# Kernel optimization log

Hardware: AMD Instinct MI355X
Metric: run time of the kernel (lower is better)

The kernel has to match this reference:

```python
import jax, jax.numpy as jnp
import numpy as np

N, E, R, F, HD = 4096, 2048, 4, 128, 256
DEG_EPS = 1e-8
BN_EPS = 1e-5
LN_EPS = 1e-5


def _xavier(k, shape):
    scale = np.sqrt(2.0 / (shape[-2] + shape[-1])).astype(np.float32)
    return jax.random.normal(k, shape, jnp.float32) * scale


def setup_inputs() -> dict:
    key = jax.random.key(0)
    ks = jax.random.split(key, 8)
    X = jax.random.normal(ks[0], (N, F), jnp.float32)
    # sparse binary incidence matrices, one per relation type, stacked [R,N,E]
    H = (jax.random.uniform(ks[1], (R, N, E)) < 0.05).astype(jnp.float32)
    return {
        "X": X,
        "H": H,
        "W1": _xavier(ks[2], (R, F, HD)),
        "W2": _xavier(ks[3], (R, HD, HD)),
        "W3": _xavier(ks[4], (R, HD, F)),
        "imp": jnp.ones((3, R), jnp.float32),        # relation_importance per conv layer
        "b1": jnp.zeros((HD,), jnp.float32),
        "b2": jnp.zeros((HD,), jnp.float32),
        "b3": jnp.zeros((F,), jnp.float32),
        "bn_gamma": jnp.ones((2, HD), jnp.float32),
        "bn_beta": jnp.zeros((2, HD), jnp.float32),
        "ln_gamma": jnp.ones((2, HD), jnp.float32),
        "ln_beta": jnp.zeros((2, HD), jnp.float32),
        "rel_attn": jnp.ones((R,), jnp.float32) / R,
    }


def typed_conv(X, Hw, W, imp, bias):
    # Hw: [R,N,E] weighted incidence; theta = Dv^{-1/2} H De^{-1/2} via row/col scaling
    dv = jnp.power(Hw.sum(axis=2) + DEG_EPS, -0.5)   # [R,N]
    de = jnp.power(Hw.sum(axis=1) + DEG_EPS, -0.5)   # [R,E]
    theta = Hw * dv[:, :, None] * de[:, None, :]     # [R,N,E]
    # (theta @ theta^T) @ X computed as theta @ (theta^T @ X) -- same math, no NxN
    t = jnp.einsum('rne,nf->ref', theta, X)          # [R,E,Fin]
    Hn = jnp.einsum('rne,ref->rnf', theta, t)        # [R,N,Fin]
    out = jnp.einsum('rnf,rfo->rno', Hn, W)          # [R,N,Fout]
    out = out * jax.nn.sigmoid(imp)[:, None, None]
    return out.sum(axis=0) + bias


def bn_ln_elu(X, bg, bb, lg, lb):
    # BatchNorm1d with batch statistics (biased var), then LayerNorm, then ELU
    mu = X.mean(axis=0)
    var = X.var(axis=0)
    X = (X - mu) * jax.lax.rsqrt(var + BN_EPS) * bg + bb
    m = X.mean(axis=-1, keepdims=True)
    v = X.var(axis=-1, keepdims=True)
    X = (X - m) * jax.lax.rsqrt(v + LN_EPS) * lg + lb
    return jax.nn.elu(X)


def reference(X, H, W1, W2, W3, imp, b1, b2, b3, bn_gamma, bn_beta, ln_gamma, ln_beta, rel_attn):
    rw = jax.nn.softmax(rel_attn)
    Hw = H * rw[:, None, None]                       # weighted incidence per relation
    h = typed_conv(X, Hw, W1, imp[0], b1)
    h = bn_ln_elu(h, bn_gamma[0], bn_beta[0], ln_gamma[0], ln_beta[0])
    h = typed_conv(h, Hw, W2, imp[1], b2)
    h = bn_ln_elu(h, bn_gamma[1], bn_beta[1], ln_gamma[1], ln_beta[1])
    out = typed_conv(h, Hw, W3, imp[2], b3)
    return out + X  # residual: out_channels == in_channels by construction
```

## Files before the change

kernel.cpp:

```cpp
#include <hip/hip_runtime.h>
#include <hip/hip_bf16.h>

#define NN 4096
#define EE 2048
#define RR 4
#define FF 128
#define HDD 256

typedef __attribute__((ext_vector_type(4))) float floatx4;
typedef __attribute__((ext_vector_type(8))) __bf16 bf16x8;

#define AS1 __attribute__((address_space(1)))
#define AS3 __attribute__((address_space(3)))

__device__ __forceinline__ void async16(const void* g, void* l) {
  __builtin_amdgcn_global_load_lds((const AS1 void*)(unsigned long long)(g),
                                   (AS3 void*)(unsigned int)(unsigned long long)(l),
                                   16, 0, 0);
}

__device__ inline unsigned short f2b(float x) {
  unsigned int u = __float_as_uint(x);
  unsigned int r = u + 0x7fffu + ((u >> 16) & 1u);
  return (unsigned short)(r >> 16);
}
__device__ inline float b2f(unsigned short u) { return __uint_as_float((unsigned int)u << 16); }

__device__ inline float rel_w(const float* rel, int r) {
  float m = fmaxf(fmaxf(rel[0], rel[1]), fmaxf(rel[2], rel[3]));
  float s = 0.f;
#pragma unroll
  for (int i = 0; i < RR; i++) s += expf(rel[i] - m);
  return expf(rel[r] - m) / s;
}

__global__ void k_prep1(const float* __restrict__ H, const float* __restrict__ rel,
                        const float* __restrict__ W1, const float* __restrict__ W2,
                        const float* __restrict__ W3, const float* __restrict__ imp,
                        float* __restrict__ dvs, unsigned long long* __restrict__ mask,
                        unsigned short* __restrict__ W1catT, unsigned short* __restrict__ W2T,
                        unsigned short* __restrict__ W3T, float* __restrict__ de, float* __restrict__ cs) {
  int b = blockIdx.x;
  if (b < 4096) {
    int wave = (b << 2) | (threadIdx.x >> 6);
    int lane = threadIdx.x & 63;
    int r = wave >> 12;
    const float* row = H + (size_t)wave * EE;
    unsigned long long* mrow = mask + (size_t)wave * (EE / 64);
    float s = 0.f;
    for (int j = 0; j < EE / 64; j++) {
      float h = row[j * 64 + lane];
      s += h;
      unsigned long long m = __ballot(h != 0.0f);
      if (lane == 0) mrow[j] = m;
    }
    for (int off = 32; off; off >>= 1) s += __shfl_down(s, off);
    if (lane == 0) {
      float rwr = rel_w(rel, r);
      dvs[wave] = rwr * rsqrtf(rwr * s + 1e-8f);
    }
  } else if (b < 4096 + 2048) {
    int idx = (b - 4096) * 256 + threadIdx.x;
    if (idx < RR * FF * HDD) {
      int o = idx % HDD, f = (idx / HDD) % FF, r = idx / (HDD * FF);
      float sg = 1.0f / (1.0f + expf(-imp[r]));
      W1catT[(size_t)o * (RR * FF) + r * FF + f] = f2b(sg * W1[((size_t)r * FF + f) * HDD + o]);
    } else if (idx < RR * FF * HDD + RR * HDD * HDD) {
      int j = idx - RR * FF * HDD;
      int c = j % HDD, o = (j / HDD) % HDD, r = j / (HDD * HDD);
      float sg = 1.0f / (1.0f + expf(-imp[RR + r]));
      W2T[j] = f2b(sg * W2[((size_t)r * HDD + c) * HDD + o]);
    } else {
      int j = idx - RR * FF * HDD - RR * HDD * HDD;
      int c = j % HDD, o = (j / HDD) % FF, r = j / (HDD * FF);
      float sg = 1.0f / (1.0f + expf(-imp[2 * RR + r]));
      W3T[j] = f2b(sg * W3[((size_t)r * HDD + c) * FF + o]);
    }
  } else {
    int i = (b - 6144) * 256 + threadIdx.x;
    if (i < RR * EE) de[i] = 0.f;
    else if (i < RR * EE + 2 * HDD) cs[i - RR * EE] = 0.f;
  }
}

__global__ void k_prep2(const unsigned long long* __restrict__ m1, unsigned long long* __restrict__ m2,
                        float* __restrict__ de, const float* __restrict__ X,
                        const float* __restrict__ dvs, unsigned short* __restrict__ XdvT) {
  __shared__ unsigned long long w[64 * 33];
  __shared__ unsigned short tile[64][65];
  int t = threadIdx.x;
  if (blockIdx.x < 256) {
    int r = blockIdx.x >> 6;
    int n0 = (blockIdx.x & 63) << 6;
    const unsigned long long* src = m1 + ((size_t)r * NN + n0) * 32;
#pragma unroll
    for (int i = 0; i < 8; i++) {
      int idx = t + i * 256;
      int n = idx >> 5, W = idx & 31;
      w[n * 33 + W] = src[idx];
    }
    __syncthreads();
    int wid = t >> 6, lane = t & 63;
    int v = n0 >> 6;
#pragma unroll
    for (int Wi = 0; Wi < 8; Wi++) {
      int W = wid * 8 + Wi;
      unsigned long long myw = w[lane * 33 + W];
      unsigned long long out = 0;
      for (int b = 0; b < 64; b++) {
        unsigned long long mm = __ballot(((myw >> b) & 1ULL) != 0);
        if (lane == b) out = mm;
      }
      m2[((size_t)r * EE + W * 64 + lane) * 64 + v] = out;
      atomicAdd(&de[r * EE + W * 64 + lane], (float)__popcll(out));
    }
  } else {
    int idx = blockIdx.x - 256;
    int c0 = (idx & 1) * 64, m0 = ((idx >> 1) & 63) * 64, r = idx >> 7;
    int tr = t >> 4, tc = t & 15;
#pragma unroll
    for (int i = 0; i < 4; i++) {
      int m = m0 + tr + 16 * i;
      float d = dvs[(size_t)r * NN + m];
      float4 v = *(const float4*)(X + (size_t)m * FF + c0 + tc * 4);
      tile[tr + 16 * i][tc * 4 + 0] = f2b(v.x * d);
      tile[tr + 16 * i][tc * 4 + 1] = f2b(v.y * d);
      tile[tr + 16 * i][tc * 4 + 2] = f2b(v.z * d);
      tile[tr + 16 * i][tc * 4 + 3] = f2b(v.w * d);
    }
    __syncthreads();
    unsigned short* db = XdvT + (size_t)r * FF * NN;
#pragma unroll
    for (int i = 0; i < 4; i++) {
      int c = c0 + tr + 16 * i;
      ushort4 v;
      v.x = tile[tc * 4 + 0][tr + 16 * i];
      v.y = tile[tc * 4 + 1][tr + 16 * i];
      v.z = tile[tc * 4 + 2][tr + 16 * i];
      v.w = tile[tc * 4 + 3][tr + 16 * i];
      *(ushort4*)(db + (size_t)c * NN + m0 + tc * 4) = v;
    }
  }
}

template <int DECA, int DECB>
__global__ __launch_bounds__(256) void k_gemm3(
    const unsigned short* __restrict__ A, const unsigned short* __restrict__ BT,
    int K, int SK, int lda, int ldb, long a_rs, long b_rs,
    unsigned short* __restrict__ P, long c_ps, long c_rs, int ldc,
    const unsigned long long* __restrict__ dm, int dnw, long drow_rs,
    const float* __restrict__ cscale, long cs_rs) {
  __shared__ unsigned short Al[2][128 * 64];
  __shared__ unsigned short Bl[2][128 * 64];
  int tid = threadIdx.x, wid = tid >> 6, lane = tid & 63;
  int m0 = blockIdx.x << 7, n0 = blockIdx.y << 7;
  int z = blockIdx.z, zr = z / SK, kz = z - zr * SK;
  int Kc = K / SK;
  int r8 = lane >> 3, c8 = lane & 7;
  int swz = ((c8 ^ r8) << 3);
  const unsigned short* Ab = A + (DECA ? 0 : ((size_t)zr * a_rs + (size_t)m0 * lda + (size_t)kz * Kc));
  const unsigned short* Bb = BT + (DECB ? 0 : ((size_t)zr * b_rs + (size_t)n0 * ldb + (size_t)kz * Kc));
  const unsigned int* mrow = nullptr;
  int drow = 0, dhalf = 0, dsw = 0;
  if (DECA || DECB) {
    drow = tid >> 1; dhalf = tid & 1;
    long mrowOff = (long)zr * drow_rs + (DECA ? m0 : n0) + drow;
    mrow = (const unsigned int*)(dm + (size_t)mrowOff * dnw);
    dsw = drow & 7;
  }
  auto stage = [&](int pb, int k0) {
    if (!DECA) {
#pragma unroll
      for (int t = 0; t < 4; t++) {
        int rbase = (wid << 5) + (t << 3);
        int row = rbase + r8;
        async16(Ab + (size_t)row * lda + k0 + swz, &Al[pb][rbase * 64 + lane * 8]);
      }
    }
    if (!DECB) {
#pragma unroll
      for (int t = 0; t < 4; t++) {
        int rbase = (wid << 5) + (t << 3);
        int row = rbase + r8;
        async16(Bb + (size_t)row * ldb + k0 + swz, &Bl[pb][rbase * 64 + lane * 8]);
      }
    }
    if (DECA || DECB) {
      unsigned short* Dl = DECA ? &Al[pb][0] : &Bl[pb][0];
      long kglob = (long)kz * Kc + k0;
      unsigned int bits = mrow[(kglob >> 5) + dhalf];
      uint4 zz = {0u, 0u, 0u, 0u};
#pragma unroll
      for (int g = 0; g < 4; g++) {
        int chunk = ((dhalf << 2) | g) ^ dsw;
        *(uint4*)&Dl[drow * 64 + chunk * 8] = zz;
      }
      while (bits) {
        int b = __builtin_ctz(bits);
        bits &= bits - 1;
        int kl = (dhalf << 5) + b;
        Dl[drow * 64 + (((kl >> 3) ^ dsw) << 3) + (kl & 7)] = (unsigned short)0x3F80;
      }
    }
  };
  int wm = (wid >> 1) << 6, wn = (wid & 1) << 6;
  int fm = lane & 15, quad = lane >> 4;
  int f7 = fm & 7;
  floatx4 acc[4][4];
#pragma unroll
  for (int i = 0; i < 4; i++)
#pragma unroll
    for (int j = 0; j < 4; j++) acc[i][j] = (floatx4){0.f, 0.f, 0.f, 0.f};
  auto compute = [&](int pb) {
#pragma unroll
    for (int ks = 0; ks < 2; ks++) {
      int kg = (ks << 2) | quad;
      int ko = ((kg ^ f7) << 3);
      bf16x8 a[4], b[4];
#pragma unroll
      for (int i = 0; i < 4; i++) {
        a[i] = *(const bf16x8*)&Al[pb][(wm + i * 16 + fm) * 64 + ko];
        b[i] = *(const bf16x8*)&Bl[pb][(wn + i * 16 + fm) * 64 + ko];
      }
#pragma unroll
      for (int i = 0; i < 4; i++)
#pragma unroll
        for (int j = 0; j < 4; j++)
          acc[i][j] = __builtin_amdgcn_mfma_f32_16x16x32_bf16(a[i], b[j], acc[i][j], 0, 0, 0);
    }
  };
  stage(0, 0);
  __syncthreads();
  for (int k0 = 0; k0 < Kc; k0 += 128) {
    if (k0 + 64 < Kc) stage(1, k0 + 64);
    compute(0);
    __syncthreads();
    if (k0 + 128 < Kc) stage(0, k0 + 128);
    compute(1);
    __syncthreads();
  }
  unsigned short* Cb = P + (size_t)kz * c_ps + (size_t)zr * c_rs;
  float csc[4];
#pragma unroll
  for (int ni = 0; ni < 4; ni++)
    csc[ni] = cscale ? cscale[(size_t)zr * cs_rs + n0 + wn + ni * 16 + fm] : 1.0f;
#pragma unroll
  for (int mi = 0; mi < 4; mi++)
#pragma unroll
    for (int ni = 0; ni < 4; ni++)
#pragma unroll
      for (int v = 0; v < 4; v++) {
        int row = m0 + wm + mi * 16 + quad * 4 + v;
        int col = n0 + wn + ni * 16 + fm;
        Cb[(size_t)row * ldc + col] = f2b(acc[mi][ni][v] * csc[ni]);
      }
}

__global__ void k_red_b(const unsigned short* __restrict__ P, unsigned short* __restrict__ out,
                        int SK, long region, const float* __restrict__ de,
                        const float* __restrict__ rel, float* __restrict__ cszero) {
  if (cszero && blockIdx.x == 0 && blockIdx.y == 0) {
    cszero[threadIdx.x] = 0.f;
    cszero[threadIdx.x + 256] = 0.f;
  }
  long i = ((long)blockIdx.x * 256 + threadIdx.x) * 8;
  int zr = blockIdx.y;
  const unsigned short* p = P + (size_t)zr * SK * region + i;
  float s[8] = {0, 0, 0, 0, 0, 0, 0, 0};
  for (int k = 0; k < SK; k++) {
    const unsigned short* q = p + (size_t)k * region;
    ushort4 a = *(const ushort4*)q;
    ushort4 b = *(const ushort4*)(q + 4);
    s[0] += b2f(a.x); s[1] += b2f(a.y); s[2] += b2f(a.z); s[3] += b2f(a.w);
    s[4] += b2f(b.x); s[5] += b2f(b.y); s[6] += b2f(b.z); s[7] += b2f(b.w);
  }
  float rwr = rel_w(rel, zr);
  int e0 = (int)(i & (EE - 1));
  float scl[8];
#pragma unroll
  for (int j = 0; j < 8; j++) scl[j] = 1.0f / (rwr * de[zr * EE + e0 + j] + 1e-8f);
  ushort4 o0, o1;
  o0.x = f2b(s[0] * scl[0]); o0.y = f2b(s[1] * scl[1]); o0.z = f2b(s[2] * scl[2]); o0.w = f2b(s[3] * scl[3]);
  o1.x = f2b(s[4] * scl[4]); o1.y = f2b(s[5] * scl[5]); o1.z = f2b(s[6] * scl[6]); o1.w = f2b(s[7] * scl[7]);
  unsigned short* d = out + (size_t)zr * region + i;
  *(ushort4*)d = o0;
  *(ushort4*)(d + 4) = o1;
}

__global__ void k_red_hcatb(const unsigned short* __restrict__ P, unsigned short* __restrict__ out,
                            int SK, const float* __restrict__ dvs) {
  long i = ((long)blockIdx.x * 256 + threadIdx.x) * 8;
  int r = blockIdx.y;
  const unsigned short* p = P + (size_t)r * SK * (NN * FF) + i;
  float s[8] = {0, 0, 0, 0, 0, 0, 0, 0};
  for (int k = 0; k < SK; k++) {
    const unsigned short* q = p + (size_t)k * (NN * FF);
    ushort4 a = *(const ushort4*)q;
    ushort4 b = *(const ushort4*)(q + 4);
    s[0] += b2f(a.x); s[1] += b2f(a.y); s[2] += b2f(a.z); s[3] += b2f(a.w);
    s[4] += b2f(b.x); s[5] += b2f(b.y); s[6] += b2f(b.z); s[7] += b2f(b.w);
  }
  long n = i >> 7;
  int f = (int)(i & 127);
  float dv = dvs[(size_t)r * NN + n];
  ushort4 o0, o1;
  o0.x = f2b(s[0] * dv); o0.y = f2b(s[1] * dv); o0.z = f2b(s[2] * dv); o0.w = f2b(s[3] * dv);
  o1.x = f2b(s[4] * dv); o1.y = f2b(s[5] * dv); o1.z = f2b(s[6] * dv); o1.w = f2b(s[7] * dv);
  unsigned short* d = out + n * (RR * FF) + r * FF + f;
  *(ushort4*)d = o0;
  *(ushort4*)(d + 4) = o1;
}

__global__ void k_redstats(const unsigned short* __restrict__ P, float* __restrict__ out,
                           float* __restrict__ cs, float* __restrict__ cs2, int Z,
                           const float* __restrict__ rs, int rshift) {
  __shared__ float sm[2][8][256];
  int cg = (threadIdx.x & 31) << 3;
  int rowt = threadIdx.x >> 5;
  int r0 = blockIdx.x * 32;
  float s[8] = {0, 0, 0, 0, 0, 0, 0, 0}, s2[8] = {0, 0, 0, 0, 0, 0, 0, 0};
  for (int j = 0; j < 4; j++) {
    int row = r0 + rowt * 4 + j;
    long idx = (long)row * HDD + cg;
    float acc[8] = {0, 0, 0, 0, 0, 0, 0, 0};
    for (int z = 0; z < Z; z++) {
      const unsigned short* p = P + (size_t)z * ((long)NN * HDD) + idx;
      float w_ = rs ? rs[(size_t)(z >> rshift) * NN + row] : 1.0f;
      ushort4 a = *(const ushort4*)p;
      ushort4 b = *(const ushort4*)(p + 4);
      acc[0] += b2f(a.x) * w_; acc[1] += b2f(a.y) * w_; acc[2] += b2f(a.z) * w_; acc[3] += b2f(a.w) * w_;
      acc[4] += b2f(b.x) * w_; acc[5] += b2f(b.y) * w_; acc[6] += b2f(b.z) * w_; acc[7] += b2f(b.w) * w_;
    }
    float4 o0 = {acc[0], acc[1], acc[2], acc[3]};
    float4 o1 = {acc[4], acc[5], acc[6], acc[7]};
    *(float4*)(out + idx) = o0;
    *(float4*)(out + idx + 4) = o1;
#pragma unroll
    for (int i = 0; i < 8; i++) { s[i] += acc[i]; s2[i] += acc[i] * acc[i]; }
  }
#pragma unroll
  for (int i = 0; i < 8; i++) { sm[0][rowt][cg + i] = s[i]; sm[1][rowt][cg + i] = s2[i]; }
  __syncthreads();
  int c = threadIdx.x;
  float a0 = 0, a1 = 0;
#pragma unroll
  for (int t = 0; t < 8; t++) { a0 += sm[0][t][c]; a1 += sm[1][t][c]; }
  atomicAdd(&cs[c], a0);
  atomicAdd(&cs2[c], a1);
}

__global__ void k_red_out(const unsigned short* __restrict__ P, const float* __restrict__ X,
                          const float* __restrict__ b3, float* __restrict__ out, int Z,
                          const float* __restrict__ rs) {
  long i = ((long)blockIdx.x * 256 + threadIdx.x) * 4;
  long n = i >> 7;
  int f = (int)(i & 127);
  float4 s = *(const float4*)(X + i);
  s.x += b3[f]; s.y += b3[f + 1]; s.z += b3[f + 2]; s.w += b3[f + 3];
  for (int z = 0; z < Z; z++) {
    float w_ = rs[(size_t)(z >> 1) * NN + n];
    ushort4 v = *(const ushort4*)(P + (size_t)z * (NN * FF) + i);
    s.x += b2f(v.x) * w_; s.y += b2f(v.y) * w_; s.z += b2f(v.z) * w_; s.w += b2f(v.w) * w_;
  }
  *(float4*)(out + i) = s;
}

__global__ void k_bnlnelu(const float* __restrict__ x, const float* __restrict__ cs, const float* __restrict__ cs2,
                          const float* __restrict__ bg, const float* __restrict__ bb,
                          const float* __restrict__ lg, const float* __restrict__ lb,
                          unsigned short* __restrict__ out) {
  int wid = threadIdx.x >> 6, lane = threadIdx.x & 63;
  int n = blockIdx.x * 4 + wid;
  float y[4];
  float m = 0.f;
#pragma unroll
  for (int j = 0; j < 4; j++) {
    int c = lane + 64 * j;
    float mu = cs[c] * (1.0f / NN);
    float var = cs2[c] * (1.0f / NN) - mu * mu;
    float xv = x[(size_t)n * HDD + c];
    y[j] = (xv - mu) * rsqrtf(var + 1e-5f) * bg[c] + bb[c];
    m += y[j];
  }
  for (int off = 32; off; off >>= 1) m += __shfl_down(m, off);
  m = __shfl(m, 0) * (1.0f / HDD);
  float var = 0.f;
#pragma unroll
  for (int j = 0; j < 4; j++) { float d = y[j] - m; var += d * d; }
  for (int off = 32; off; off >>= 1) var += __shfl_down(var, off);
  var = __shfl(var, 0) * (1.0f / HDD);
  float inv = rsqrtf(var + 1e-5f);
#pragma unroll
  for (int j = 0; j < 4; j++) {
    int c = lane + 64 * j;
    float z = (y[j] - m) * inv * lg[c] + lb[c];
    z = z > 0.f ? z : expm1f(z);
    out[(size_t)n * HDD + c] = f2b(z);
  }
}

extern "C" void kernel_launch(void* const* d_in, const int* in_sizes, int n_in,
                              void* d_out, int out_size, void* d_ws, size_t ws_size,
                              hipStream_t stream) {
  const float* X   = (const float*)d_in[0];
  const float* H   = (const float*)d_in[1];
  const float* W1  = (const float*)d_in[2];
  const float* W2  = (const float*)d_in[3];
  const float* W3  = (const float*)d_in[4];
  const float* imp = (const float*)d_in[5];
  const float* b3  = (const float*)d_in[8];
  const float* bng = (const float*)d_in[9];
  const float* bnb = (const float*)d_in[10];
  const float* lng = (const float*)d_in[11];
  const float* lnb = (const float*)d_in[12];
  const float* rel = (const float*)d_in[13];
  (void)in_sizes; (void)n_in; (void)out_size; (void)ws_size;

  char* w = (char*)d_ws;
  size_t off = 0;
  auto alloc = [&](size_t bytes) -> void* {
    void* p = w + off;
    off += (bytes + 255) & ~(size_t)255;
    return p;
  };
  float* dvs  = (float*)alloc((size_t)RR * NN * 4);
  float* de   = (float*)alloc((size_t)RR * EE * 4);
  float* cs   = (float*)alloc(2 * HDD * 4);
  unsigned long long* mask1 = (unsigned long long*)alloc((size_t)RR * NN * (EE / 64) * 8);
  unsigned long long* mask2 = (unsigned long long*)alloc((size_t)RR * EE * (NN / 64) * 8);
  unsigned short* bufP = (unsigned short*)alloc((size_t)16 * NN * HDD * 2);
  unsigned short* bufC = (unsigned short*)alloc((size_t)RR * EE * HDD * 2);
  unsigned short* bufD = (unsigned short*)alloc((size_t)RR * EE * HDD * 2);
  unsigned short* bufE = (unsigned short*)alloc((size_t)RR * EE * HDD * 2);
  float* convout = (float*)alloc((size_t)NN * HDD * 4);
  unsigned short* Xb    = (unsigned short*)alloc((size_t)NN * HDD * 2);
  unsigned short* XdvT  = (unsigned short*)alloc((size_t)RR * FF * NN * 2);
  unsigned short* hwdvT = (unsigned short*)alloc((size_t)RR * HDD * NN * 2);
  unsigned short* W1catT = (unsigned short*)alloc((size_t)RR * FF * HDD * 2);
  unsigned short* W2T    = (unsigned short*)alloc((size_t)RR * HDD * HDD * 2);
  unsigned short* W3T    = (unsigned short*)alloc((size_t)RR * HDD * FF * 2);

  k_prep1<<<4096 + 2048 + 34, 256, 0, stream>>>(H, rel, W1, W2, W3, imp,
                                                dvs, mask1, W1catT, W2T, W3T, de, cs);
  k_prep2<<<256 + 512, 256, 0, stream>>>(mask1, mask2, de, X, dvs, XdvT);

  k_gemm3<0, 1><<<dim3(1, EE / 128, RR * 8), 256, 0, stream>>>(
      XdvT, nullptr, NN, 8, NN, 0, (long)FF * NN, 0,
      bufP, (long)FF * EE, 8L * FF * EE, EE, mask2, NN / 64, EE, nullptr, 0);
  k_red_b<<<dim3((FF * EE) / 2048, RR), 256, 0, stream>>>(
      bufP, bufC, 8, (long)FF * EE, de, rel, nullptr);
  k_gemm3<1, 0><<<dim3(NN / 128, 1, RR * 2), 256, 0, stream>>>(
      nullptr, bufC, EE, 2, 0, EE, 0, (long)FF * EE,
      bufP, (long)NN * FF, 2L * NN * FF, FF, mask1, EE / 64, NN, nullptr, 0);
  k_red_hcatb<<<dim3((NN * FF) / 2048, RR), 256, 0, stream>>>(bufP, bufD, 2, dvs);
  k_gemm3<0, 0><<<dim3(NN / 128, HDD / 128, 4), 256, 0, stream>>>(
      bufD, W1catT, RR * FF, 4, RR * FF, RR * FF, 0, 0,
      bufP, (long)NN * HDD, 0, HDD, nullptr, 0, 0, nullptr, 0);
  k_redstats<<<NN / 32, 256, 0, stream>>>(bufP, convout, cs, cs + HDD, 4, nullptr, 0);
  k_bnlnelu<<<NN / 4, 256, 0, stream>>>(convout, cs, cs + HDD, bng, bnb, lng, lnb, Xb);

  k_gemm3<0, 0><<<dim3(HDD / 128, NN / 128, RR), 256, 0, stream>>>(
      W2T, Xb, HDD, 1, HDD, HDD, (long)HDD * HDD, 0,
      hwdvT, 0, (long)HDD * NN, NN, nullptr, 0, 0, dvs, NN);
  k_gemm3<0, 1><<<dim3(HDD / 128, EE / 128, RR * 4), 256, 0, stream>>>(
      hwdvT, nullptr, NN, 4, NN, 0, (long)HDD * NN, 0,
      bufP, (long)HDD * EE, 4L * HDD * EE, EE, mask2, NN / 64, EE, nullptr, 0);
  k_red_b<<<dim3((HDD * EE) / 2048, RR), 256, 0, stream>>>(
      bufP, bufE, 4, (long)HDD * EE, de, rel, cs);
  k_gemm3<1, 0><<<dim3(NN / 128, HDD / 128, RR * 2), 256, 0, stream>>>(
      nullptr, bufE, EE, 2, 0, EE, 0, (long)HDD * EE,
      bufP, (long)NN * HDD, 2L * NN * HDD, HDD, mask1, EE / 64, NN, nullptr, 0);
  k_redstats<<<NN / 32, 256, 0, stream>>>(bufP, convout, cs, cs + HDD, 8, dvs, 1);
  k_bnlnelu<<<NN / 4, 256, 0, stream>>>(convout, cs, cs + HDD, bng + HDD, bnb + HDD, lng + HDD, lnb + HDD, Xb);

  k_gemm3<0, 0><<<dim3(1, NN / 128, RR), 256, 0, stream>>>(
      W3T, Xb, HDD, 1, HDD, HDD, (long)FF * HDD, 0,
      bufD, 0, (long)FF * NN, NN, nullptr, 0, 0, dvs, NN);
  k_gemm3<0, 1><<<dim3(1, EE / 128, RR * 8), 256, 0, stream>>>(
      bufD, nullptr, NN, 8, NN, 0, (long)FF * NN, 0,
      bufP, (long)FF * EE, 8L * FF * EE, EE, mask2, NN / 64, EE, nullptr, 0);
  k_red_b<<<dim3((FF * EE) / 2048, RR), 256, 0, stream>>>(
      bufP, bufC, 8, (long)FF * EE, de, rel, nullptr);
  k_gemm3<1, 0><<<dim3(NN / 128, 1, RR * 2), 256, 0, stream>>>(
      nullptr, bufC, EE, 2, 0, EE, 0, (long)FF * EE,
      bufP, (long)NN * FF, 2L * NN * FF, FF, mask1, EE / 64, NN, nullptr, 0);
  k_red_out<<<(NN * FF) / 1024, 256, 0, stream>>>(bufP, X, b3, (float*)d_out, 8, dvs);
}
```

Before: 470.1 us.

## Flatten relation sum into K dimension and fold degree scales into GEMM

Each second-stage incidence GEMM now spans all relations by concatenating relations along K (R*E). The dv scaling is baked into the decoded incidence values instead of a constant 1.0, so the cross-relation sum happens inside the MFMA accumulation rather than in separate per-relation reductions. Layer 1 is reordered to apply W1 on the edge side (E rows instead of N), and the de scaling moves into the GEMM epilogue. This removes the k_red_hcatb kernel and the weighted reductions. In exchange, dv is stored in bf16 inside the decoded tiles and the layouts and split-K counts change.

Measured after the change: 490.6 us. 4.4% more time.

```diff
diff --git a/kernel.cpp b/kernel.cpp
--- a/kernel.cpp
+++ b/kernel.cpp
@@ -143,13 +143,16 @@
   }
 }
 
-template <int DECA, int DECB>
+template <int DEC, int FLAT>
 __global__ __launch_bounds__(256) void k_gemm3(
     const unsigned short* __restrict__ A, const unsigned short* __restrict__ BT,
     int K, int SK, int lda, int ldb, long a_rs, long b_rs,
     unsigned short* __restrict__ P, long c_ps, long c_rs, int ldc,
     const unsigned long long* __restrict__ dm, int dnw, long drow_rs,
-    const float* __restrict__ cscale, long cs_rs) {
+    const float* __restrict__ dvs_,
+    const float* __restrict__ cscale, long cs_rs,
+    const float* __restrict__ derow, const float* __restrict__ decol,
+    const float* __restrict__ rel) {
   __shared__ unsigned short Al[2][128 * 64];
   __shared__ unsigned short Bl[2][128 * 64];
   int tid = threadIdx.x, wid = tid >> 6, lane = tid & 63;
@@ -158,18 +161,26 @@
   int Kc = K / SK;
   int r8 = lane >> 3, c8 = lane & 7;
   int swz = ((c8 ^ r8) << 3);
-  const unsigned short* Ab = A + (DECA ? 0 : ((size_t)zr * a_rs + (size_t)m0 * lda + (size_t)kz * Kc));
-  const unsigned short* Bb = BT + (DECB ? 0 : ((size_t)zr * b_rs + (size_t)n0 * ldb + (size_t)kz * Kc));
+  const unsigned short* Ab = A + (DEC == 1 ? 0 : ((size_t)zr * a_rs + (size_t)m0 * lda + (size_t)kz * Kc));
+  const unsigned short* Bb = BT + (DEC == 2 ? 0 : ((size_t)zr * b_rs + (size_t)n0 * ldb + (size_t)kz * Kc));
   const unsigned int* mrow = nullptr;
   int drow = 0, dhalf = 0, dsw = 0;
-  if (DECA || DECB) {
+  unsigned long long dvpack = 0;
+  if (DEC) {
     drow = tid >> 1; dhalf = tid & 1;
-    long mrowOff = (long)zr * drow_rs + (DECA ? m0 : n0) + drow;
-    mrow = (const unsigned int*)(dm + (size_t)mrowOff * dnw);
     dsw = drow & 7;
+    if (FLAT) {
+      int n = m0 + drow;
+#pragma unroll
+      for (int r4 = 0; r4 < 4; r4++)
+        dvpack |= (unsigned long long)f2b(dvs_[(r4 << 12) + n]) << (r4 << 4);
+    } else {
+      long mrowOff = (long)zr * drow_rs + (DEC == 1 ? m0 : n0) + drow;
+      mrow = (const unsigned int*)(dm + (size_t)mrowOff * dnw);
+    }
   }
   auto stage = [&](int pb, int k0) {
-    if (!DECA) {
+    if (DEC != 1) {
 #pragma unroll
       for (int t = 0; t < 4; t++) {
         int rbase = (wid << 5) + (t << 3);
@@ -177,7 +188,7 @@
         async16(Ab + (size_t)row * lda + k0 + swz, &Al[pb][rbase * 64 + lane * 8]);
       }
     }
-    if (!DECB) {
+    if (DEC != 2) {
 #pragma unroll
       for (int t = 0; t < 4; t++) {
         int rbase = (wid << 5) + (t << 3);
@@ -185,10 +196,20 @@
         async16(Bb + (size_t)row * ldb + k0 + swz, &Bl[pb][rbase * 64 + lane * 8]);
       }
     }
-    if (DECA || DECB) {
-      unsigned short* Dl = DECA ? &Al[pb][0] : &Bl[pb][0];
+    if (DEC) {
+      unsigned short* Dl = (DEC == 1) ? &Al[pb][0] : &Bl[pb][0];
       long kglob = (long)kz * Kc + k0;
-      unsigned int bits = mrow[(kglob >> 5) + dhalf];
+      unsigned int bits;
+      unsigned short sval;
+      if (FLAT) {
+        int rr = (int)(kglob >> 11);
+        int ew = (((int)kglob) & 2047) >> 5;
+        bits = ((const unsigned int*)dm)[(((size_t)rr << 12) + (size_t)(m0 + drow)) * 64 + ew + dhalf];
+        sval = (unsigned short)(dvpack >> ((rr & 3) << 4));
+      } else {
+        bits = mrow[(kglob >> 5) + dhalf];
+        sval = (unsigned short)0x3F80;
+      }
       uint4 zz = {0u, 0u, 0u, 0u};
 #pragma unroll
       for (int g = 0; g < 4; g++) {
@@ -199,7 +220,7 @@
         int b = __builtin_ctz(bits);
         bits &= bits - 1;
         int kl = (dhalf << 5) + b;
-        Dl[drow * 64 + (((kl >> 3) ^ dsw) << 3) + (kl & 7)] = (unsigned short)0x3F80;
+        Dl[drow * 64 + (((kl >> 3) ^ dsw) << 3) + (kl & 7)] = sval;
       }
     }
   };
@@ -240,10 +261,16 @@
     __syncthreads();
   }
   unsigned short* Cb = P + (size_t)kz * c_ps + (size_t)zr * c_rs;
+  float rwr = (derow || decol) ? rel_w(rel, zr) : 0.f;
   float csc[4];
 #pragma unroll
-  for (int ni = 0; ni < 4; ni++)
-    csc[ni] = cscale ? cscale[(size_t)zr * cs_rs + n0 + wn + ni * 16 + fm] : 1.0f;
+  for (int ni = 0; ni < 4; ni++) {
+    int col = n0 + wn + ni * 16 + fm;
+    float c = 1.0f;
+    if (cscale) c = cscale[(size_t)zr * cs_rs + col];
+    if (decol) c = 1.0f / (rwr * decol[(size_t)zr * EE + col] + 1e-8f);
+    csc[ni] = c;
+  }
 #pragma unroll
   for (int mi = 0; mi < 4; mi++)
 #pragma unroll
@@ -252,13 +279,14 @@
       for (int v = 0; v < 4; v++) {
         int row = m0 + wm + mi * 16 + quad * 4 + v;
         int col = n0 + wn + ni * 16 + fm;
-        Cb[(size_t)row * ldc + col] = f2b(acc[mi][ni][v] * csc[ni]);
+        float val = acc[mi][ni][v] * csc[ni];
+        if (derow) val *= 1.0f / (rwr * derow[(size_t)zr * EE + row] + 1e-8f);
+        Cb[(size_t)row * ldc + col] = f2b(val);
       }
 }
 
 __global__ void k_red_b(const unsigned short* __restrict__ P, unsigned short* __restrict__ out,
-                        int SK, long region, const float* __restrict__ de,
-                        const float* __restrict__ rel, float* __restrict__ cszero) {
+                        int SK, long region, float* __restrict__ cszero) {
   if (cszero && blockIdx.x == 0 && blockIdx.y == 0) {
     cszero[threadIdx.x] = 0.f;
     cszero[threadIdx.x + 256] = 0.f;
@@ -274,46 +302,16 @@
     s[0] += b2f(a.x); s[1] += b2f(a.y); s[2] += b2f(a.z); s[3] += b2f(a.w);
     s[4] += b2f(b.x); s[5] += b2f(b.y); s[6] += b2f(b.z); s[7] += b2f(b.w);
   }
-  float rwr = rel_w(rel, zr);
-  int e0 = (int)(i & (EE - 1));
-  float scl[8];
-#pragma unroll
-  for (int j = 0; j < 8; j++) scl[j] = 1.0f / (rwr * de[zr * EE + e0 + j] + 1e-8f);
   ushort4 o0, o1;
-  o0.x = f2b(s[0] * scl[0]); o0.y = f2b(s[1] * scl[1]); o0.z = f2b(s[2] * scl[2]); o0.w = f2b(s[3] * scl[3]);
-  o1.x = f2b(s[4] * scl[4]); o1.y = f2b(s[5] * scl[5]); o1.z = f2b(s[6] * scl[6]); o1.w = f2b(s[7] * scl[7]);
+  o0.x = f2b(s[0]); o0.y = f2b(s[1]); o0.z = f2b(s[2]); o0.w = f2b(s[3]);
+  o1.x = f2b(s[4]); o1.y = f2b(s[5]); o1.z = f2b(s[6]); o1.w = f2b(s[7]);
   unsigned short* d = out + (size_t)zr * region + i;
   *(ushort4*)d = o0;
   *(ushort4*)(d + 4) = o1;
 }
 
-__global__ void k_red_hcatb(const unsigned short* __restrict__ P, unsigned short* __restrict__ out,
-                            int SK, const float* __restrict__ dvs) {
-  long i = ((long)blockIdx.x * 256 + threadIdx.x) * 8;
-  int r = blockIdx.y;
-  const unsigned short* p = P + (size_t)r * SK * (NN * FF) + i;
-  float s[8] = {0, 0, 0, 0, 0, 0, 0, 0};
-  for (int k = 0; k < SK; k++) {
-    const unsigned short* q = p + (size_t)k * (NN * FF);
-    ushort4 a = *(const ushort4*)q;
-    ushort4 b = *(const ushort4*)(q + 4);
-    s[0] += b2f(a.x); s[1] += b2f(a.y); s[2] += b2f(a.z); s[3] += b2f(a.w);
-    s[4] += b2f(b.x); s[5] += b2f(b.y); s[6] += b2f(b.z); s[7] += b2f(b.w);
-  }
-  long n = i >> 7;
-  int f = (int)(i & 127);
-  float dv = dvs[(size_t)r * NN + n];
-  ushort4 o0, o1;
-  o0.x = f2b(s[0] * dv); o0.y = f2b(s[1] * dv); o0.z = f2b(s[2] * dv); o0.w = f2b(s[3] * dv);
-  o1.x = f2b(s[4] * dv); o1.y = f2b(s[5] * dv); o1.z = f2b(s[6] * dv); o1.w = f2b(s[7] * dv);
-  unsigned short* d = out + n * (RR * FF) + r * FF + f;
-  *(ushort4*)d = o0;
-  *(ushort4*)(d + 4) = o1;
-}
-
 __global__ void k_redstats(const unsigned short* __restrict__ P, float* __restrict__ out,
-                           float* __restrict__ cs, float* __restrict__ cs2, int Z,
-                           const float* __restrict__ rs, int rshift) {
+                           float* __restrict__ cs, float* __restrict__ cs2, int Z) {
   __shared__ float sm[2][8][256];
   int cg = (threadIdx.x & 31) << 3;
   int rowt = threadIdx.x >> 5;
@@ -325,11 +323,10 @@
     float acc[8] = {0, 0, 0, 0, 0, 0, 0, 0};
     for (int z = 0; z < Z; z++) {
       const unsigned short* p = P + (size_t)z * ((long)NN * HDD) + idx;
-      float w_ = rs ? rs[(size_t)(z >> rshift) * NN + row] : 1.0f;
       ushort4 a = *(const ushort4*)p;
       ushort4 b = *(const ushort4*)(p + 4);
-      acc[0] += b2f(a.x) * w_; acc[1] += b2f(a.y) * w_; acc[2] += b2f(a.z) * w_; acc[3] += b2f(a.w) * w_;
-      acc[4] += b2f(b.x) * w_; acc[5] += b2f(b.y) * w_; acc[6] += b2f(b.z) * w_; acc[7] += b2f(b.w) * w_;
+      acc[0] += b2f(a.x); acc[1] += b2f(a.y); acc[2] += b2f(a.z); acc[3] += b2f(a.w);
+      acc[4] += b2f(b.x); acc[5] += b2f(b.y); acc[6] += b2f(b.z); acc[7] += b2f(b.w);
     }
     float4 o0 = {acc[0], acc[1], acc[2], acc[3]};
     float4 o1 = {acc[4], acc[5], acc[6], acc[7]};
@@ -350,17 +347,14 @@
 }
 
 __global__ void k_red_out(const unsigned short* __restrict__ P, const float* __restrict__ X,
-                          const float* __restrict__ b3, float* __restrict__ out, int Z,
-                          const float* __restrict__ rs) {
+                          const float* __restrict__ b3, float* __restrict__ out, int Z) {
   long i = ((long)blockIdx.x * 256 + threadIdx.x) * 4;
-  long n = i >> 7;
   int f = (int)(i & 127);
   float4 s = *(const float4*)(X + i);
   s.x += b3[f]; s.y += b3[f + 1]; s.z += b3[f + 2]; s.w += b3[f + 3];
   for (int z = 0; z < Z; z++) {
-    float w_ = rs[(size_t)(z >> 1) * NN + n];
     ushort4 v = *(const ushort4*)(P + (size_t)z * (NN * FF) + i);
-    s.x += b2f(v.x) * w_; s.y += b2f(v.y) * w_; s.z += b2f(v.z) * w_; s.w += b2f(v.w) * w_;
+    s.x += b2f(v.x); s.y += b2f(v.y); s.z += b2f(v.z); s.w += b2f(v.w);
   }
   *(float4*)(out + i) = s;
 }
@@ -439,50 +433,61 @@
   unsigned short* W1catT = (unsigned short*)alloc((size_t)RR * FF * HDD * 2);
   unsigned short* W2T    = (unsigned short*)alloc((size_t)RR * HDD * HDD * 2);
   unsigned short* W3T    = (unsigned short*)alloc((size_t)RR * HDD * FF * 2);
+  unsigned short* Z1T  = bufD;
+  unsigned short* bufE2 = bufE;
+  unsigned short* ydvT = XdvT;
+  unsigned short* bufC2 = bufC;
 
   k_prep1<<<4096 + 2048 + 34, 256, 0, stream>>>(H, rel, W1, W2, W3, imp,
                                                 dvs, mask1, W1catT, W2T, W3T, de, cs);
   k_prep2<<<256 + 512, 256, 0, stream>>>(mask1, mask2, de, X, dvs, XdvT);
 
-  k_gemm3<0, 1><<<dim3(1, EE / 128, RR * 8), 256, 0, stream>>>(
-      XdvT, nullptr, NN, 8, NN, 0, (long)FF * NN, 0,
-      bufP, (long)FF * EE, 8L * FF * EE, EE, mask2, NN / 64, EE, nullptr, 0);
-  k_red_b<<<dim3((FF * EE) / 2048, RR), 256, 0, stream>>>(
-      bufP, bufC, 8, (long)FF * EE, de, rel, nullptr);
-  k_gemm3<1, 0><<<dim3(NN / 128, 1, RR * 2), 256, 0, stream>>>(
-      nullptr, bufC, EE, 2, 0, EE, 0, (long)FF * EE,
-      bufP, (long)NN * FF, 2L * NN * FF, FF, mask1, EE / 64, NN, nullptr, 0);
-  k_red_hcatb<<<dim3((NN * FF) / 2048, RR), 256, 0, stream>>>(bufP, bufD, 2, dvs);
-  k_gemm3<0, 0><<<dim3(NN / 128, HDD / 128, 4), 256, 0, stream>>>(
-      bufD, W1catT, RR * FF, 4, RR * FF, RR * FF, 0, 0,
-      bufP, (long)NN * HDD, 0, HDD, nullptr, 0, 0, nullptr, 0);
-  k_redstats<<<NN / 32, 256, 0, stream>>>(bufP, convout, cs, cs + HDD, 4, nullptr, 0);
+  k_gemm3<1, 0><<<dim3(EE / 128, 1, RR * 8), 256, 0, stream>>>(
+      nullptr, XdvT, NN, 8, 0, NN, 0, (long)FF * NN,
+      bufP, (long)EE * FF, 8L * EE * FF, FF,
+      mask2, NN / 64, EE, nullptr, nullptr, 0, de, nullptr, rel);
+  k_red_b<<<dim3((EE * FF) / 2048, RR), 256, 0, stream>>>(bufP, bufC, 8, (long)EE * FF, nullptr);
+  k_gemm3<0, 0><<<dim3(HDD / 128, EE / 128, RR), 256, 0, stream>>>(
+      W1catT, bufC, FF, 1, RR * FF, FF, FF, (long)EE * FF,
+      Z1T, 0, EE, RR * EE,
+      nullptr, 0, 0, nullptr, nullptr, 0, nullptr, nullptr, nullptr);
+  k_gemm3<1, 1><<<dim3(NN / 128, HDD / 128, 8), 256, 0, stream>>>(
+      nullptr, Z1T, RR * EE, 8, 0, RR * EE, 0, 0,
+      bufP, (long)NN * HDD, 0, HDD,
+      mask1, 0, 0, dvs, nullptr, 0, nullptr, nullptr, nullptr);
+  k_redstats<<<NN / 32, 256, 0, stream>>>(bufP, convout, cs, cs + HDD, 8);
   k_bnlnelu<<<NN / 4, 256, 0, stream>>>(convout, cs, cs + HDD, bng, bnb, lng, lnb, Xb);
 
   k_gemm3<0, 0><<<dim3(HDD / 128, NN / 128, RR), 256, 0, stream>>>(
       W2T, Xb, HDD, 1, HDD, HDD, (long)HDD * HDD, 0,
-      hwdvT, 0, (long)HDD * NN, NN, nullptr, 0, 0, dvs, NN);
-  k_gemm3<0, 1><<<dim3(HDD / 128, EE / 128, RR * 4), 256, 0, stream>>>(
+      hwdvT, 0, (long)HDD * NN, NN,
+      nullptr, 0, 0, nullptr, dvs, NN, nullptr, nullptr, nullptr);
+  k_gemm3<2, 0><<<dim3(HDD / 128, EE / 128, RR * 4), 256, 0, stream>>>(
       hwdvT, nullptr, NN, 4, NN, 0, (long)HDD * NN, 0,
-      bufP, (long)HDD * EE, 4L * HDD * EE, EE, mask2, NN / 64, EE, nullptr, 0);
-  k_red_b<<<dim3((HDD * EE) / 2048, RR), 256, 0, stream>>>(
-      bufP, bufE, 4, (long)HDD * EE, de, rel, cs);
-  k_gemm3<1, 0><<<dim3(NN / 128, HDD / 128, RR * 2), 256, 0, stream>>>(
-      nullptr, bufE, EE, 2, 0, EE, 0, (long)HDD * EE,
-      bufP, (long)NN * HDD, 2L * NN * HDD, HDD, mask1, EE / 64, NN, nullptr, 0);
-  k_redstats<<<NN / 32, 256, 0, stream>>>(bufP, convout, cs, cs + HDD, 8, dvs, 1);
+      bufP, (long)HDD * RR * EE, EE, RR * EE,
+      mask2, NN / 64, EE, nullptr, nullptr, 0, nullptr, de, rel);
+  k_red_b<<<dim3((HDD * RR * EE) / 2048, 1), 256, 0, stream>>>(
+      bufP, bufE2, 4, (long)HDD * RR * EE, cs);
+  k_gemm3<1, 1><<<dim3(NN / 128, HDD / 128, 8), 256, 0, stream>>>(
+      nullptr, bufE2, RR * EE, 8, 0, RR * EE, 0, 0,
+      bufP, (long)NN * HDD, 0, HDD,
+      mask1, 0, 0, dvs, nullptr, 0, nullptr, nullptr, nullptr);
+  k_redstats<<<NN / 32, 256, 0, stream>>>(bufP, convout, cs, cs + HDD, 8);
   k_bnlnelu<<<NN / 4, 256, 0, stream>>>(convout, cs, cs + HDD, bng + HDD, bnb + HDD, lng + HDD, lnb + HDD, Xb);
 
   k_gemm3<0, 0><<<dim3(1, NN / 128, RR), 256, 0, stream>>>(
       W3T, Xb, HDD, 1, HDD, HDD, (long)FF * HDD, 0,
-      bufD, 0, (long)FF * NN, NN, nullptr, 0, 0, dvs, NN);
-  k_gemm3<0, 1><<<dim3(1, EE / 128, RR * 8), 256, 0, stream>>>(
-      bufD, nullptr, NN, 8, NN, 0, (long)FF * NN, 0,
-      bufP, (long)FF * EE, 8L * FF * EE, EE, mask2, NN / 64, EE, nullptr, 0);
-  k_red_b<<<dim3((FF * EE) / 2048, RR), 256, 0, stream>>>(
-      bufP, bufC, 8, (long)FF * EE, de, rel, nullptr);
-  k_gemm3<1, 0><<<dim3(NN / 128, 1, RR * 2), 256, 0, stream>>>(
-      nullptr, bufC, EE, 2, 0, EE, 0, (long)FF * EE,
-      bufP, (long)NN * FF, 2L * NN * FF, FF, mask1, EE / 64, NN, nullptr, 0);
-  k_red_out<<<(NN * FF) / 1024, 256, 0, stream>>>(bufP, X, b3, (float*)d_out, 8, dvs);
-}
+      ydvT, 0, (long)FF * NN, NN,
+      nullptr, 0, 0, nullptr, dvs, NN, nullptr, nullptr, nullptr);
+  k_gemm3<2, 0><<<dim3(1, EE / 128, RR * 8), 256, 0, stream>>>(
+      ydvT, nullptr, NN, 8, NN, 0, (long)FF * NN, 0,
+      bufP, (long)FF * RR * EE, EE, RR * EE,
+      mask2, NN / 64, EE, nullptr, nullptr, 0, nullptr, de, rel);
+  k_red_b<<<dim3((FF * RR * EE) / 2048, 1), 256, 0, stream>>>(
+      bufP, bufC2, 8, (long)FF * RR * EE, nullptr);
+  k_gemm3<1, 1><<<dim3(NN / 128, 1, 16), 256, 0, stream>>>(
+      nullptr, bufC2, RR * EE, 16, 0, RR * EE, 0, 0,
+      bufP, (long)NN * FF, 0, FF,
+      mask1, 0, 0, dvs, nullptr, 0, nullptr, nullptr, nullptr);
+  k_red_out<<<(NN * FF) / 1024, 256, 0, stream>>>(bufP, X, b3, (float*)d_out, 16);
+}
```

## Vectorize mask build with permuted edge order, raise split-K for node-side GEMMs

Applied to the files above, without the earlier changes.

The incidence scan in k_prep1 now reads H as float4 and issues four ballots per load. This permutes the edge bit order in mask1, and mask2 and de are re-indexed to match. The decode for the A-side bitmask GEMM is rewritten to gather the permuted bits, which adds per-tile decoding work. The N-side GEMMs for the 128-wide layers use split-K 4 instead of 2 to get more blocks in flight, and the reductions and buffer reuse (XdvT instead of bufD) are adjusted to fit. The cost is a larger partial-sum reduction.

Result: no change. 477.3 us (+1.5%).

```diff
diff --git a/kernel.cpp b/kernel.cpp
--- a/kernel.cpp
+++ b/kernel.cpp
@@ -45,14 +45,23 @@
     int wave = (b << 2) | (threadIdx.x >> 6);
     int lane = threadIdx.x & 63;
     int r = wave >> 12;
-    const float* row = H + (size_t)wave * EE;
-    unsigned long long* mrow = mask + (size_t)wave * (EE / 64);
+    const float4* row = (const float4*)(H + (size_t)wave * EE);
+    unsigned long long* mrow = mask + (size_t)wave * 32;
     float s = 0.f;
-    for (int j = 0; j < EE / 64; j++) {
-      float h = row[j * 64 + lane];
-      s += h;
-      unsigned long long m = __ballot(h != 0.0f);
-      if (lane == 0) mrow[j] = m;
+#pragma unroll
+    for (int jj = 0; jj < 8; jj++) {
+      float4 v = row[jj * 64 + lane];
+      s += v.x + v.y + v.z + v.w;
+      unsigned long long m0 = __ballot(v.x != 0.0f);
+      unsigned long long m1 = __ballot(v.y != 0.0f);
+      unsigned long long m2 = __ballot(v.z != 0.0f);
+      unsigned long long m3 = __ballot(v.w != 0.0f);
+      if (lane == 0) {
+        mrow[jj * 4 + 0] = m0;
+        mrow[jj * 4 + 1] = m1;
+        mrow[jj * 4 + 2] = m2;
+        mrow[jj * 4 + 3] = m3;
+      }
     }
     for (int off = 32; off; off >>= 1) s += __shfl_down(s, off);
     if (lane == 0) {
@@ -92,7 +101,7 @@
   if (blockIdx.x < 256) {
     int r = blockIdx.x >> 6;
     int n0 = (blockIdx.x & 63) << 6;
-    const unsigned long long* src = m1 + ((size_t)r * NN + n0) * 32;
+    const unsigned long long* src = m1 + ((size_t)(r << 12) + n0) * 32;
 #pragma unroll
     for (int i = 0; i < 8; i++) {
       int idx = t + i * 256;
@@ -107,12 +116,13 @@
       int W = wid * 8 + Wi;
       unsigned long long myw = w[lane * 33 + W];
       unsigned long long out = 0;
-      for (int b = 0; b < 64; b++) {
-        unsigned long long mm = __ballot(((myw >> b) & 1ULL) != 0);
-        if (lane == b) out = mm;
-      }
-      m2[((size_t)r * EE + W * 64 + lane) * 64 + v] = out;
-      atomicAdd(&de[r * EE + W * 64 + lane], (float)__popcll(out));
+      for (int bb = 0; bb < 64; bb++) {
+        unsigned long long mm = __ballot(((myw >> bb) & 1ull) != 0);
+        if (lane == bb) out = mm;
+      }
+      int e = ((W >> 2) << 8) + (lane << 2) + (W & 3);
+      m2[((size_t)r * EE + e) * 64 + v] = out;
+      atomicAdd(&de[r * EE + e], (float)__popcll(out));
     }
   } else {
     int idx = blockIdx.x - 256;
@@ -188,18 +198,35 @@
     if (DECA || DECB) {
       unsigned short* Dl = DECA ? &Al[pb][0] : &Bl[pb][0];
       long kglob = (long)kz * Kc + k0;
-      unsigned int bits = mrow[(kglob >> 5) + dhalf];
       uint4 zz = {0u, 0u, 0u, 0u};
 #pragma unroll
       for (int g = 0; g < 4; g++) {
         int chunk = ((dhalf << 2) | g) ^ dsw;
         *(uint4*)&Dl[drow * 64 + chunk * 8] = zz;
       }
-      while (bits) {
-        int b = __builtin_ctz(bits);
-        bits &= bits - 1;
-        int kl = (dhalf << 5) + b;
-        Dl[drow * 64 + (((kl >> 3) ^ dsw) << 3) + (kl & 7)] = (unsigned short)0x3F80;
+      if (DECA) {
+        int jj = (int)(kglob >> 8);
+        int lbase = (((int)kglob & 255) >> 2) + (dhalf << 3);
+        int u32sel = lbase >> 5, sh = lbase & 31;
+#pragma unroll
+        for (int c = 0; c < 4; c++) {
+          unsigned int wbits = mrow[(((jj << 2) + c) << 1) + u32sel];
+          unsigned int bb = (wbits >> sh) & 0xffu;
+          while (bb) {
+            int b = __builtin_ctz(bb);
+            bb &= bb - 1;
+            int kl = (((dhalf << 3) + b) << 2) | c;
+            Dl[drow * 64 + (((kl >> 3) ^ dsw) << 3) + (kl & 7)] = (unsigned short)0x3F80;
+          }
+        }
+      } else {
+        unsigned int bits = mrow[(kglob >> 5) + dhalf];
+        while (bits) {
+          int b = __builtin_ctz(bits);
+          bits &= bits - 1;
+          int kl = (dhalf << 5) + b;
+          Dl[drow * 64 + (((kl >> 3) ^ dsw) << 3) + (kl & 7)] = (unsigned short)0x3F80;
+        }
       }
     }
   };
@@ -351,14 +378,14 @@
 
 __global__ void k_red_out(const unsigned short* __restrict__ P, const float* __restrict__ X,
                           const float* __restrict__ b3, float* __restrict__ out, int Z,
-                          const float* __restrict__ rs) {
+                          const float* __restrict__ rs, int rshift) {
   long i = ((long)blockIdx.x * 256 + threadIdx.x) * 4;
   long n = i >> 7;
   int f = (int)(i & 127);
   float4 s = *(const float4*)(X + i);
   s.x += b3[f]; s.y += b3[f + 1]; s.z += b3[f + 2]; s.w += b3[f + 3];
   for (int z = 0; z < Z; z++) {
-    float w_ = rs[(size_t)(z >> 1) * NN + n];
+    float w_ = rs[(size_t)(z >> rshift) * NN + n];
     ushort4 v = *(const ushort4*)(P + (size_t)z * (NN * FF) + i);
     s.x += b2f(v.x) * w_; s.y += b2f(v.y) * w_; s.z += b2f(v.z) * w_; s.w += b2f(v.w) * w_;
   }
@@ -426,8 +453,8 @@
   float* dvs  = (float*)alloc((size_t)RR * NN * 4);
   float* de   = (float*)alloc((size_t)RR * EE * 4);
   float* cs   = (float*)alloc(2 * HDD * 4);
-  unsigned long long* mask1 = (unsigned long long*)alloc((size_t)RR * NN * (EE / 64) * 8);
-  unsigned long long* mask2 = (unsigned long long*)alloc((size_t)RR * EE * (NN / 64) * 8);
+  unsigned long long* mask1 = (unsigned long long*)alloc((size_t)RR * NN * 32 * 8);
+  unsigned long long* mask2 = (unsigned long long*)alloc((size_t)RR * EE * 64 * 8);
   unsigned short* bufP = (unsigned short*)alloc((size_t)16 * NN * HDD * 2);
   unsigned short* bufC = (unsigned short*)alloc((size_t)RR * EE * HDD * 2);
   unsigned short* bufD = (unsigned short*)alloc((size_t)RR * EE * HDD * 2);
@@ -449,10 +476,10 @@
       bufP, (long)FF * EE, 8L * FF * EE, EE, mask2, NN / 64, EE, nullptr, 0);
   k_red_b<<<dim3((FF * EE) / 2048, RR), 256, 0, stream>>>(
       bufP, bufC, 8, (long)FF * EE, de, rel, nullptr);
-  k_gemm3<1, 0><<<dim3(NN / 128, 1, RR * 2), 256, 0, stream>>>(
-      nullptr, bufC, EE, 2, 0, EE, 0, (long)FF * EE,
-      bufP, (long)NN * FF, 2L * NN * FF, FF, mask1, EE / 64, NN, nullptr, 0);
-  k_red_hcatb<<<dim3((NN * FF) / 2048, RR), 256, 0, stream>>>(bufP, bufD, 2, dvs);
+  k_gemm3<1, 0><<<dim3(NN / 128, 1, RR * 4), 256, 0, stream>>>(
+      nullptr, bufC, EE, 4, 0, EE, 0, (long)FF * EE,
+      bufP, (long)NN * FF, 4L * NN * FF, FF, mask1, EE / 64, NN, nullptr, 0);
+  k_red_hcatb<<<dim3((NN * FF) / 2048, RR), 256, 0, stream>>>(bufP, bufD, 4, dvs);
   k_gemm3<0, 0><<<dim3(NN / 128, HDD / 128, 4), 256, 0, stream>>>(
       bufD, W1catT, RR * FF, 4, RR * FF, RR * FF, 0, 0,
       bufP, (long)NN * HDD, 0, HDD, nullptr, 0, 0, nullptr, 0);
@@ -475,14 +502,14 @@
 
   k_gemm3<0, 0><<<dim3(1, NN / 128, RR), 256, 0, stream>>>(
       W3T, Xb, HDD, 1, HDD, HDD, (long)FF * HDD, 0,
-      bufD, 0, (long)FF * NN, NN, nullptr, 0, 0, dvs, NN);
+      XdvT, 0, (long)FF * NN, NN, nullptr, 0, 0, dvs, NN);
   k_gemm3<0, 1><<<dim3(1, EE / 128, RR * 8), 256, 0, stream>>>(
-      bufD, nullptr, NN, 8, NN, 0, (long)FF * NN, 0,
+      XdvT, nullptr, NN, 8, NN, 0, (long)FF * NN, 0,
       bufP, (long)FF * EE, 8L * FF * EE, EE, mask2, NN / 64, EE, nullptr, 0);
   k_red_b<<<dim3((FF * EE) / 2048, RR), 256, 0, stream>>>(
       bufP, bufC, 8, (long)FF * EE, de, rel, nullptr);
-  k_gemm3<1, 0><<<dim3(NN / 128, 1, RR * 2), 256, 0, stream>>>(
-      nullptr, bufC, EE, 2, 0, EE, 0, (long)FF * EE,
-      bufP, (long)NN * FF, 2L * NN * FF, FF, mask1, EE / 64, NN, nullptr, 0);
-  k_red_out<<<(NN * FF) / 1024, 256, 0, stream>>>(bufP, X, b3, (float*)d_out, 8, dvs);
-}
+  k_gemm3<1, 0><<<dim3(NN / 128, 1, RR * 4), 256, 0, stream>>>(
+      nullptr, bufC, EE, 4, 0, EE, 0, (long)FF * EE,
+      bufP, (long)NN * FF, 4L * NN * FF, FF, mask1, EE / 64, NN, nullptr, 0);
+  k_red_out<<<(NN * FF) / 1024, 256, 0, stream>>>(bufP, X, b3, (float*)d_out, 16, dvs, 2);
+}
```
